# Kernel optimization log

Hardware: AMD Instinct MI355X
Metric: run time of the kernel (lower is better)

Reference implementation:

```python
import jax, jax.numpy as jnp
import numpy as np

N = 50000      # nodes
E = 800000     # edges
H = 64         # hidden_dim
T = 32         # max_node_types
G = 256        # graphs in batch
EPS = 1e-5


def gcn_conv(x, src, dst, W, b, n):
    # GCNConv: transform, add self-loops, symmetric deg normalization, scatter-sum
    x = x @ W  # [N, C]
    loops = jnp.arange(n)
    row = jnp.concatenate([src, loops])
    col = jnp.concatenate([dst, loops])
    deg = jax.ops.segment_sum(jnp.ones_like(col, dtype=x.dtype), col, num_segments=n)
    dinv = jnp.where(deg > 0, jax.lax.rsqrt(deg), 0.0)
    norm = dinv[row] * dinv[col]  # [E+N]
    out = jax.ops.segment_sum(x[row] * norm[:, None], col, num_segments=n)
    return out + b


def batchnorm(x, gamma, beta):
    mean = x.mean(axis=0)
    var = x.var(axis=0)
    return (x - mean) * jax.lax.rsqrt(var + EPS) * gamma + beta


def setup_inputs() -> dict:
    key = jax.random.key(0)
    ks = jax.random.split(key, 24)
    s = 0.05
    nrm = lambda k, shape: (jax.random.normal(k, shape, dtype=jnp.float32) * s)
    inp = {
        "type_ids": jax.random.randint(ks[0], (N,), 0, T),
        "c": jax.random.normal(ks[1], (N,), dtype=jnp.float32),
        "gm": jax.random.normal(ks[2], (N,), dtype=jnp.float32),
        "pos": jax.random.normal(ks[3], (N,), dtype=jnp.float32),
        "r": jax.random.normal(ks[4], (N,), dtype=jnp.float32),
        "vid": jax.random.normal(ks[5], (N,), dtype=jnp.float32),
        "edge_index": jax.random.randint(ks[6], (2, E), 0, N),
        "batch_idx": jnp.sort(jax.random.randint(ks[7], (N,), 0, G)),
        "W1": nrm(ks[8], (T, H)), "b1": jnp.zeros((H,), jnp.float32),
        "W2": nrm(ks[9], (5, H)), "b2": jnp.zeros((H,), jnp.float32),
        "Wg0": nrm(ks[10], (2 * H, H)), "bg0": jnp.zeros((H,), jnp.float32),
        "Wg1": nrm(ks[11], (H, H)), "bg1": jnp.zeros((H,), jnp.float32),
        "Wg2": nrm(ks[12], (H, H)), "bg2": jnp.zeros((H,), jnp.float32),
        "gam0": jnp.ones((H,), jnp.float32), "bet0": jnp.zeros((H,), jnp.float32),
        "gam1": jnp.ones((H,), jnp.float32), "bet1": jnp.zeros((H,), jnp.float32),
        "Wout": nrm(ks[13], (H, 4)), "bout": jnp.zeros((4,), jnp.float32),
    }
    return inp


def reference(type_ids, c, gm, pos, r, vid, edge_index, batch_idx,
              W1, b1, W2, b2, Wg0, bg0, Wg1, bg1, Wg2, bg2,
              gam0, bet0, gam1, bet1, Wout, bout):
    # OneHot embedding branch
    x_t = jax.nn.one_hot(type_ids, T, dtype=jnp.float32) @ W1 + b1   # [N, H]
    x_num = jnp.stack([c, gm, pos, r, vid], axis=-1) @ W2 + b2       # [N, H]
    z = jnp.concatenate([x_t, x_num], axis=-1)                       # [N, 2H]
    src, dst = edge_index[0], edge_index[1]
    # GCN (PyG BasicGNN): conv -> bn -> relu for first L-1 layers, last conv bare
    z = gcn_conv(z, src, dst, Wg0, bg0, N)
    z = jax.nn.relu(batchnorm(z, gam0, bet0))
    z = gcn_conv(z, src, dst, Wg1, bg1, N)
    z = jax.nn.relu(batchnorm(z, gam1, bet1))
    z = gcn_conv(z, src, dst, Wg2, bg2, N)
    # outer activation
    z = jax.nn.relu(z)
    # global_mean_pool over batch index
    sums = jax.ops.segment_sum(z, batch_idx, num_segments=G)
    counts = jax.ops.segment_sum(jnp.ones((N,), jnp.float32), batch_idx, num_segments=G)
    pooled = sums / jnp.maximum(counts, 1.0)[:, None]                # [G, H]
    return pooled @ Wout + bout                                      # [G, 4]
```

## Files before the change

### kernel.cpp

```cpp
#include <hip/hip_runtime.h>
#include <hip/hip_bf16.h>


__device__ __forceinline__ unsigned short f2bf(float f) {
    unsigned int x = (unsigned int)__float_as_int(f);
    x += 0x7fffu + ((x >> 16) & 1u);
    return (unsigned short)(x >> 16);
}

#define CONV_BLOCKS 1024

__global__ void precompute_mats(const float* __restrict__ W1, const float* __restrict__ b1,
                                const float* __restrict__ W2, const float* __restrict__ b2,
                                const float* __restrict__ Wg0,
                                float* __restrict__ M1, float* __restrict__ M2,
                                float* __restrict__ cvec, int T) {
    int tid = threadIdx.x;
    for (int idx = tid; idx < T * 64; idx += blockDim.x) {
        int t = idx >> 6, c = idx & 63;
        float a = 0.f;
        for (int k = 0; k < 64; ++k) a += W1[t * 64 + k] * Wg0[k * 64 + c];
        M1[idx] = a;
    }
    for (int idx = tid; idx < 5 * 64; idx += blockDim.x) {
        int j = idx >> 6, c = idx & 63;
        float a = 0.f;
        for (int k = 0; k < 64; ++k) a += W2[j * 64 + k] * Wg0[(64 + k) * 64 + c];
        M2[idx] = a;
    }
    for (int c = tid; c < 64; c += blockDim.x) {
        float a = 0.f;
        for (int k = 0; k < 64; ++k)
            a += b1[k] * Wg0[k * 64 + c] + b2[k] * Wg0[(64 + k) * 64 + c];
        cvec[c] = a;
    }
}

__global__ void node_embed(const int* __restrict__ type_ids,
                           const float* __restrict__ f0, const float* __restrict__ f1,
                           const float* __restrict__ f2, const float* __restrict__ f3,
                           const float* __restrict__ f4,
                           const float* __restrict__ M1, const float* __restrict__ M2,
                           const float* __restrict__ cvec, const float* __restrict__ dinv,
                           unsigned short* __restrict__ hb, int n) {
    int i = blockIdx.x * (blockDim.x >> 6) + (threadIdx.x >> 6);
    int lane = threadIdx.x & 63;
    if (i >= n) return;
    int t = type_ids[i];
    float a = M1[t * 64 + lane] + cvec[lane];
    a += f0[i] * M2[0 * 64 + lane];
    a += f1[i] * M2[1 * 64 + lane];
    a += f2[i] * M2[2 * 64 + lane];
    a += f3[i] * M2[3 * 64 + lane];
    a += f4[i] * M2[4 * 64 + lane];
    hb[((unsigned)i << 6) | lane] = f2bf(a * dinv[i]);
}

__global__ void count_deg(const int* __restrict__ dst, int* __restrict__ deg, int e) {
    int i = blockIdx.x * blockDim.x + threadIdx.x;
    if (i < e) atomicAdd(&deg[dst[i]], 1);
}

#define SCAN_TILE 1024
__global__ void scan_local(const int* __restrict__ deg, int* __restrict__ loc,
                           int* __restrict__ tilesum, float* __restrict__ dinv, int n) {
    __shared__ int wsum[16];
    __shared__ int wexcl[16];
    const int tid = threadIdx.x;
    const int lane = tid & 63, w = tid >> 6;
    int i = blockIdx.x * SCAN_TILE + tid;
    int v = (i < n) ? deg[i] : 0;
    if (i < n) dinv[i] = rsqrtf((float)(v + 1));
    int incl = v;
#pragma unroll
    for (int ofs = 1; ofs < 64; ofs <<= 1) {
        int t = __shfl_up(incl, (unsigned)ofs, 64);
        if (lane >= ofs) incl += t;
    }
    if (lane == 63) wsum[w] = incl;
    __syncthreads();
    if (w == 0 && lane < 16) {
        int s = wsum[lane];
        int sc = s;
#pragma unroll
        for (int ofs = 1; ofs < 16; ofs <<= 1) {
            int t = __shfl_up(sc, (unsigned)ofs, 64);
            if (lane >= ofs) sc += t;
        }
        wexcl[lane] = sc - s;
        if (lane == 15) wsum[15] = sc;
    }
    __syncthreads();
    if (i < n) loc[i] = wexcl[w] + incl;
    if (tid == 0) tilesum[blockIdx.x] = wsum[15];
}

__global__ void scan_tiles(int* __restrict__ tilesum, int* __restrict__ tileoff, int nt) {
    int lane = threadIdx.x;
    int v = (lane < nt) ? tilesum[lane] : 0;
    int incl = v;
#pragma unroll
    for (int ofs = 1; ofs < 64; ofs <<= 1) {
        int t = __shfl_up(incl, (unsigned)ofs, 64);
        if (lane >= ofs) incl += t;
    }
    if (lane < nt) tileoff[lane] = incl - v;
}

__global__ void scan_add(const int* __restrict__ loc, const int* __restrict__ tileoff,
                         int* __restrict__ off, int* __restrict__ cursor, int n) {
    int i = blockIdx.x * blockDim.x + threadIdx.x;
    if (i >= n) return;
    int val = tileoff[i / SCAN_TILE] + loc[i];
    off[i + 1] = val;
    if (i + 1 < n) cursor[i + 1] = val;
    if (i == 0) { off[0] = 0; cursor[0] = 0; }
}

#define NB 64
__global__ void init_buckets(const int* __restrict__ off, int* __restrict__ bkt_cursor,
                             int N) {
    int b = threadIdx.x;
    if (b < NB) bkt_cursor[b] = off[min(b << 10, N)];
}

#define EPB 8192
__global__ void bucket_edges(const int* __restrict__ src, const int* __restrict__ dst,
                             int* __restrict__ bkt_cursor, unsigned* __restrict__ bucketed,
                             int E) {
    __shared__ int hist[NB];
    __shared__ int base_[NB];
    const int t = threadIdx.x;
    int start = blockIdx.x * EPB;
    int end = min(E, start + EPB);
    if (t < NB) hist[t] = 0;
    __syncthreads();
    for (int i = start + t; i < end; i += 256) {
        int b = dst[i] >> 10;
        atomicAdd(&hist[b], 1);
    }
    __syncthreads();
    if (t < NB) {
        base_[t] = atomicAdd(&bkt_cursor[t], hist[t]);
        hist[t] = 0;
    }
    __syncthreads();
    for (int i = start + t; i < end; i += 256) {
        int d = dst[i];
        int b = d >> 10;
        int slot = atomicAdd(&hist[b], 1);
        bucketed[base_[b] + slot] = ((unsigned)src[i] << 16) | (unsigned)d;
    }
}

#define SCAT_SLICES 4
__global__ void scatter_csr(const unsigned* __restrict__ bucketed, const int* __restrict__ off,
                            int* __restrict__ cursor, unsigned short* __restrict__ csr_u,
                            int N) {
    int wg = blockIdx.x;
    int b = wg / SCAT_SLICES, q = wg % SCAT_SLICES;
    int bstart = off[min(b << 10, N)];
    int bend = off[min((b + 1) << 10, N)];
    int cntb = bend - bstart;
    if (cntb == 0) return;
    int per = (cntb + SCAT_SLICES - 1) / SCAT_SLICES;
    int s0 = bstart + q * per;
    int s1 = min(bend, s0 + per);
    for (int i = s0 + (int)threadIdx.x; i < s1; i += 256) {
        unsigned u = bucketed[i];
        int s = (int)(u >> 16);
        int d = (int)(u & 0xffffu);
        int pos = atomicAdd(&cursor[d], 1);
        csr_u[pos] = (unsigned short)s;
    }
}

__global__ void build_graph_off(const int* __restrict__ batch, int* __restrict__ go,
                                int n, int G) {
    int i = blockIdx.x * blockDim.x + threadIdx.x;
    if (i >= n) return;
    int b = batch[i];
    if (i == 0) {
        for (int g = 0; g <= b; ++g) go[g] = 0;
    } else {
        int p = batch[i - 1];
        if (p != b) for (int g = p + 1; g <= b; ++g) go[g] = i;
    }
    if (i == n - 1) {
        for (int g = b + 1; g <= G; ++g) go[g] = n;
    }
}

__device__ __forceinline__ void gather_add(float acc[8], uint4 v) {
    acc[0] += __uint_as_float(v.x << 16);
    acc[1] += __uint_as_float(v.x & 0xffff0000u);
    acc[2] += __uint_as_float(v.y << 16);
    acc[3] += __uint_as_float(v.y & 0xffff0000u);
    acc[4] += __uint_as_float(v.z << 16);
    acc[5] += __uint_as_float(v.z & 0xffff0000u);
    acc[6] += __uint_as_float(v.w << 16);
    acc[7] += __uint_as_float(v.w & 0xffff0000u);
}

__device__ __forceinline__ void reduce8(float acc[8]) {
#pragma unroll
    for (int q = 0; q < 8; ++q) {
        acc[q] += __shfl_xor(acc[q], 8, 64);
        acc[q] += __shfl_xor(acc[q], 16, 64);
        acc[q] += __shfl_xor(acc[q], 32, 64);
    }
}

__device__ __forceinline__ void node_aggregate(float acc[8],
                                               const unsigned short* __restrict__ hb,
                                               const unsigned short* __restrict__ csr_u,
                                               int i, int b, int deg, int N,
                                               int eg, int cc) {
#pragma unroll
    for (int q = 0; q < 8; ++q) acc[q] = 0.f;
    int nb = (deg + 8) >> 3;
#pragma unroll 1
    for (int t = 0; t < nb; t += 4) {
        int j0 = (t << 3) + eg;
        int j1 = j0 + 8, j2 = j0 + 16, j3 = j0 + 24;
        unsigned e0 = csr_u[b + j0 - 1];
        unsigned e1 = csr_u[b + j1 - 1];
        unsigned e2 = csr_u[b + j2 - 1];
        unsigned e3 = csr_u[b + j3 - 1];
        unsigned s0 = (j0 == 0) ? (unsigned)i : ((j0 <= deg) ? e0 : (unsigned)N);
        unsigned s1 = (j1 <= deg) ? e1 : (unsigned)N;
        unsigned s2 = (j2 <= deg) ? e2 : (unsigned)N;
        unsigned s3 = (j3 <= deg) ? e3 : (unsigned)N;
        uint4 v0 = *(const uint4*)&hb[(s0 << 6) + (cc << 3)];
        uint4 v1 = *(const uint4*)&hb[(s1 << 6) + (cc << 3)];
        uint4 v2 = *(const uint4*)&hb[(s2 << 6) + (cc << 3)];
        uint4 v3 = *(const uint4*)&hb[(s3 << 6) + (cc << 3)];
        gather_add(acc, v0);
        gather_add(acc, v1);
        gather_add(acc, v2);
        gather_add(acc, v3);
    }
    reduce8(acc);
}

__device__ __forceinline__ void node_aggregate_pair(float accA[8], float accB[8],
                                                    const unsigned short* __restrict__ hb,
                                                    const unsigned short* __restrict__ csr_u,
                                                    int iA, int bA, int degA,
                                                    int iB, int bB, int degB,
                                                    int N, int eg, int cc) {
#pragma unroll
    for (int q = 0; q < 8; ++q) { accA[q] = 0.f; accB[q] = 0.f; }
    int dmax = max(degA, degB);
    int nb = (dmax + 8) >> 3;
#pragma unroll 1
    for (int t = 0; t < nb; t += 2) {
        int j0 = (t << 3) + eg;
        int j1 = j0 + 8;
        unsigned a0 = csr_u[bA + j0 - 1];
        unsigned a1 = csr_u[bA + j1 - 1];
        unsigned c0 = csr_u[bB + j0 - 1];
        unsigned c1 = csr_u[bB + j1 - 1];
        unsigned sA0 = (j0 == 0) ? (unsigned)iA : ((j0 <= degA) ? a0 : (unsigned)N);
        unsigned sA1 = (j1 <= degA) ? a1 : (unsigned)N;
        unsigned sB0 = (j0 == 0) ? (unsigned)iB : ((j0 <= degB) ? c0 : (unsigned)N);
        unsigned sB1 = (j1 <= degB) ? c1 : (unsigned)N;
        uint4 vA0 = *(const uint4*)&hb[(sA0 << 6) + (cc << 3)];
        uint4 vB0 = *(const uint4*)&hb[(sB0 << 6) + (cc << 3)];
        uint4 vA1 = *(const uint4*)&hb[(sA1 << 6) + (cc << 3)];
        uint4 vB1 = *(const uint4*)&hb[(sB1 << 6) + (cc << 3)];
        gather_add(accA, vA0);
        gather_add(accB, vB0);
        gather_add(accA, vA1);
        gather_add(accB, vB1);
    }
    reduce8(accA);
    reduce8(accB);
}

__global__ __launch_bounds__(256, 2) void conv_gather_bn(
        const unsigned short* __restrict__ hb,
        const int* __restrict__ off, const unsigned short* __restrict__ csr_u,
        const float* __restrict__ dinv, const float* __restrict__ bias,
        float* __restrict__ y, float* __restrict__ partials, int n) {
    __shared__ float sh[4][128];
    const int w = threadIdx.x >> 6;
    const int lane = threadIdx.x & 63;
    const int eg = lane >> 3, cc = lane & 7;
    const int wid = blockIdx.x * 4 + w;
    const int nw = gridDim.x * 4;
    const float4* b4 = (const float4*)bias;
    float4 bb0 = b4[cc * 2], bb1 = b4[cc * 2 + 1];
    float bl[8] = {bb0.x, bb0.y, bb0.z, bb0.w, bb1.x, bb1.y, bb1.z, bb1.w};
    float bsum[8], bsq[8];
#pragma unroll
    for (int q = 0; q < 8; ++q) { bsum[q] = 0.f; bsq[q] = 0.f; }

    for (int iA = wid * 2; iA < n; iA += nw * 2) {
        int iB = iA + 1;
        bool bv = iB < n;
        int iBc = bv ? iB : iA;
        int bA = off[iA], degA = off[iA + 1] - bA;
        int bB = off[iBc], degB = off[iBc + 1] - bB;
        float accA[8], accB[8];
        node_aggregate_pair(accA, accB, hb, csr_u, iA, bA, degA, iBc, bB, degB,
                            n, eg, cc);
        if (eg == 0) {
            float diA = dinv[iA];
            float oA[8];
#pragma unroll
            for (int q = 0; q < 8; ++q) {
                oA[q] = accA[q] * diA + bl[q];
                bsum[q] += oA[q];
                bsq[q] += oA[q] * oA[q];
            }
            float4* o = (float4*)&y[((size_t)iA << 6) + (cc << 3)];
            o[0] = make_float4(oA[0], oA[1], oA[2], oA[3]);
            o[1] = make_float4(oA[4], oA[5], oA[6], oA[7]);
            if (bv) {
                float diB = dinv[iB];
                float oB[8];
#pragma unroll
                for (int q = 0; q < 8; ++q) {
                    oB[q] = accB[q] * diB + bl[q];
                    bsum[q] += oB[q];
                    bsq[q] += oB[q] * oB[q];
                }
                float4* ob = (float4*)&y[((size_t)iB << 6) + (cc << 3)];
                ob[0] = make_float4(oB[0], oB[1], oB[2], oB[3]);
                ob[1] = make_float4(oB[4], oB[5], oB[6], oB[7]);
            }
        }
    }
    if (eg == 0) {
#pragma unroll
        for (int q = 0; q < 8; ++q) {
            sh[w][cc * 8 + q] = bsum[q];
            sh[w][64 + cc * 8 + q] = bsq[q];
        }
    }
    __syncthreads();
    if (threadIdx.x < 128) {
        int t = threadIdx.x;
        partials[blockIdx.x * 128 + t] = sh[0][t] + sh[1][t] + sh[2][t] + sh[3][t];
    }
}

#define POOL_SLICES 16
__global__ __launch_bounds__(256, 2) void conv_relu_pool(
        const unsigned short* __restrict__ hb,
        const int* __restrict__ off, const unsigned short* __restrict__ csr_u,
        const float* __restrict__ dinv, const float* __restrict__ bias,
        const int* __restrict__ go, float* __restrict__ pooled, int n, int G) {
    int wave = blockIdx.x * (blockDim.x >> 6) + (threadIdx.x >> 6);
    int g = wave >> 4, k = wave & (POOL_SLICES - 1);
    if (g >= G) return;
    const int lane = threadIdx.x & 63;
    const int eg = lane >> 3, cc = lane & 7;
    int gs = go[g], ge = go[g + 1];
    int cntg = ge - gs;
    if (cntg == 0) return;
    int per = (cntg + POOL_SLICES - 1) >> 4;
    int s0 = gs + k * per;
    int s1 = min(ge, s0 + per);
    if (s0 >= s1) return;
    const float4* b4 = (const float4*)bias;
    float4 bb0 = b4[cc * 2], bb1 = b4[cc * 2 + 1];
    float bl[8] = {bb0.x, bb0.y, bb0.z, bb0.w, bb1.x, bb1.y, bb1.z, bb1.w};
    float accp[8];
#pragma unroll
    for (int q = 0; q < 8; ++q) accp[q] = 0.f;
    int i = s0;
    for (; i + 1 < s1; i += 2) {
        int bA = off[i], degA = off[i + 1] - bA;
        int bB = off[i + 1], degB = off[i + 2] - bB;
        float accA[8], accB[8];
        node_aggregate_pair(accA, accB, hb, csr_u, i, bA, degA, i + 1, bB, degB,
                            n, eg, cc);
        float diA = dinv[i], diB = dinv[i + 1];
#pragma unroll
        for (int q = 0; q < 8; ++q) {
            accp[q] += fmaxf(accA[q] * diA + bl[q], 0.f);
            accp[q] += fmaxf(accB[q] * diB + bl[q], 0.f);
        }
    }
    if (i < s1) {
        int b = off[i], deg = off[i + 1] - b;
        float acc[8];
        node_aggregate(acc, hb, csr_u, i, b, deg, n, eg, cc);
        float di = dinv[i];
#pragma unroll
        for (int q = 0; q < 8; ++q) accp[q] += fmaxf(acc[q] * di + bl[q], 0.f);
    }
    atomicAdd(&pooled[g * 64 + (cc << 3) + eg], accp[eg]);
}

__global__ __launch_bounds__(1024) void bn_finalize(const float* __restrict__ partials, int nblk,
                            const float* __restrict__ gamma, const float* __restrict__ beta,
                            float* __restrict__ scsh, int n) {
    __shared__ float red[8][128];
    __shared__ float tot[128];
    int t = threadIdx.x;
    int ch = t & 127, sl = t >> 7;
    float a = 0.f;
#pragma unroll 8
    for (int b = sl; b < nblk; b += 8) a += partials[b * 128 + ch];
    red[sl][ch] = a;
    __syncthreads();
    if (t < 128) {
        float s = 0.f;
#pragma unroll
        for (int i = 0; i < 8; ++i) s += red[i][t];
        tot[t] = s;
    }
    __syncthreads();
    if (t < 64) {
        float mean = tot[t] / (float)n;
        float var = tot[64 + t] / (float)n - mean * mean;
        float sc = rsqrtf(var + 1e-5f) * gamma[t];
        scsh[t] = sc;
        scsh[64 + t] = beta[t] - mean * sc;
    }
}

struct alignas(16) us8 { unsigned short v[8]; };
__global__ __launch_bounds__(256, 2) void bn_relu_gemm(const float* __restrict__ y,
                             const float* __restrict__ scsh, const float* __restrict__ W,
                             const float* __restrict__ dinv,
                             unsigned short* __restrict__ hb, int n) {
    __shared__ float4 yt4[128 * 16];
    __shared__ float4 wt4[64 * 16];
    float* wt = (float*)wt4;
    const int t = threadIdx.x;
    const int base = blockIdx.x * 128;

    const float4* W4 = (const float4*)W;
#pragma unroll
    for (int i = 0; i < 4; ++i) {
        int g = t + 256 * i;
        int k = g >> 4;
        int c0 = (g & 15) << 2;
        float4 wv = W4[g];
        float wvf[4] = {wv.x, wv.y, wv.z, wv.w};
#pragma unroll
        for (int j = 0; j < 4; ++j) {
            int c = c0 + j;
            wt[c * 64 + (((k >> 2) ^ ((c >> 2) & 15)) << 2) + (k & 3)] = wvf[j];
        }
    }
    const float4* y4 = (const float4*)y;
#pragma unroll
    for (int i = 0; i < 8; ++i) {
        int g = t + 256 * i;
        int r = g >> 4, kc = g & 15;
        int row = base + r;
        float4 v = make_float4(0.f, 0.f, 0.f, 0.f);
        if (row < n) v = y4[(size_t)row * 16 + kc];
        int c0 = kc << 2;
        v.x = fmaxf(v.x * scsh[c0 + 0] + scsh[64 + c0 + 0], 0.f);
        v.y = fmaxf(v.y * scsh[c0 + 1] + scsh[64 + c0 + 1], 0.f);
        v.z = fmaxf(v.z * scsh[c0 + 2] + scsh[64 + c0 + 2], 0.f);
        v.w = fmaxf(v.w * scsh[c0 + 3] + scsh[64 + c0 + 3], 0.f);
        yt4[r * 16 + (kc ^ ((r >> 2) & 15))] = v;
    }
    __syncthreads();

    const int w = t >> 6;
    const int lane = t & 63;
    const int ng = lane >> 3;
    const int cg = lane & 7;
    const int rl = w * 32 + ng * 4;
    const int c0 = cg * 8;
    const int sa = (rl >> 2) & 15;
    float acc[4][8];
#pragma unroll
    for (int m = 0; m < 4; ++m)
#pragma unroll
        for (int j = 0; j < 8; ++j) acc[m][j] = 0.f;

#pragma unroll 1
    for (int kc = 0; kc < 16; ++kc) {
        float4 a[4];
#pragma unroll
        for (int m = 0; m < 4; ++m) a[m] = yt4[(rl + m) * 16 + (kc ^ sa)];
#pragma unroll
        for (int j = 0; j < 8; ++j) {
            int c = c0 + j;
            float4 b = wt4[c * 16 + (kc ^ ((c >> 2) & 15))];
#pragma unroll
            for (int m = 0; m < 4; ++m)
                acc[m][j] += a[m].x * b.x + a[m].y * b.y +
                             a[m].z * b.z + a[m].w * b.w;
        }
    }

#pragma unroll
    for (int m = 0; m < 4; ++m) {
        int row = base + rl + m;
        if (row < n) {
            float dv = dinv[row];
            us8 p;
#pragma unroll
            for (int j = 0; j < 8; ++j) p.v[j] = f2bf(acc[m][j] * dv);
            *(us8*)&hb[((size_t)row << 6) | c0] = p;
        }
    }
}

__global__ void final_out(const float* __restrict__ pooled, const int* __restrict__ go,
                          const float* __restrict__ Wout, const float* __restrict__ bout,
                          float* __restrict__ out, int G) {
    int idx = blockIdx.x * blockDim.x + threadIdx.x;
    if (idx >= G * 4) return;
    int g = idx >> 2, o = idx & 3;
    float inv = 1.f / fmaxf((float)(go[g + 1] - go[g]), 1.f);
    float a = 0.f;
    for (int k = 0; k < 64; ++k) a += pooled[g * 64 + k] * Wout[k * 4 + o];
    out[idx] = a * inv + bout[o];
}

extern "C" void kernel_launch(void* const* d_in, const int* in_sizes, int n_in,
                              void* d_out, int out_size, void* d_ws, size_t ws_size,
                              hipStream_t stream) {
    const int N = in_sizes[0];
    const int E = in_sizes[6] / 2;
    const int T = in_sizes[8] / 64;
    const int G = out_size / 4;

    const int*   type_ids = (const int*)d_in[0];
    const float* fc   = (const float*)d_in[1];
    const float* fgm  = (const float*)d_in[2];
    const float* fpos = (const float*)d_in[3];
    const float* fr   = (const float*)d_in[4];
    const float* fvid = (const float*)d_in[5];
    const int*   ei   = (const int*)d_in[6];
    const int*   batch = (const int*)d_in[7];
    const float* W1 = (const float*)d_in[8];
    const float* b1 = (const float*)d_in[9];
    const float* W2 = (const float*)d_in[10];
    const float* b2 = (const float*)d_in[11];
    const float* Wg0 = (const float*)d_in[12];
    const float* bg0 = (const float*)d_in[13];
    const float* Wg1 = (const float*)d_in[14];
    const float* bg1 = (const float*)d_in[15];
    const float* Wg2 = (const float*)d_in[16];
    const float* bg2 = (const float*)d_in[17];
    const float* gam0 = (const float*)d_in[18];
    const float* bet0 = (const float*)d_in[19];
    const float* gam1 = (const float*)d_in[20];
    const float* bet1 = (const float*)d_in[21];
    const float* Wout = (const float*)d_in[22];
    const float* bout = (const float*)d_in[23];

    const int* e_src = ei;
    const int* e_dst = ei + E;

    char* ws = (char*)d_ws;
    size_t o = 0;
    auto alloc = [&](size_t bytes) -> char* {
        char* p = ws + o;
        o += (bytes + 255) & ~(size_t)255;
        return p;
    };
    const int NTILES = (N + SCAN_TILE - 1) / SCAN_TILE;
    unsigned short* hb = (unsigned short*)alloc((size_t)(N + 1) * 64 * 2);
    float* y        = (float*)alloc((size_t)N * 64 * 4);
    int*   deg      = (int*)alloc((size_t)N * 4);
    float* dinv     = (float*)alloc((size_t)N * 4);
    int*   off      = (int*)alloc((size_t)(N + 1) * 4);
    int*   cursor   = (int*)alloc((size_t)N * 4);
    int*   loc      = (int*)alloc((size_t)N * 4);
    int*   tilesum  = (int*)alloc((size_t)NTILES * 4);
    int*   tileoff  = (int*)alloc((size_t)NTILES * 4);
    unsigned short* csrBuf = (unsigned short*)alloc(((size_t)E + 160) * 2);
    unsigned short* csr_u  = csrBuf + 1;
    unsigned* bucketed = (unsigned*)alloc((size_t)E * 4);
    int*   bkt_cursor  = (int*)alloc(NB * 4);
    int*   go       = (int*)alloc((size_t)(G + 1) * 4);
    float* part0    = (float*)alloc((size_t)CONV_BLOCKS * 128 * 4);
    float* part1    = (float*)alloc((size_t)CONV_BLOCKS * 128 * 4);
    float* scsh0    = (float*)alloc(128 * 4);
    float* scsh1    = (float*)alloc(128 * 4);
    float* pooled   = (float*)alloc((size_t)G * 64 * 4);
    float* M1       = (float*)alloc((size_t)T * 64 * 4);
    float* M2       = (float*)alloc(5 * 64 * 4);
    float* cvec     = (float*)alloc(64 * 4);
    (void)ws_size;

    hipMemsetAsync(deg, 0, (size_t)N * 4, stream);
    hipMemsetAsync(csrBuf, 0, 2, stream);
    hipMemsetAsync(csr_u + E, 0, 128 * 2, stream);
    hipMemsetAsync(hb + (size_t)N * 64, 0, 128, stream);
    hipMemsetAsync(pooled, 0, (size_t)G * 64 * 4, stream);

    const int waves_per_blk = 4;
    const int nblk_nodes = (N + waves_per_blk - 1) / waves_per_blk;
    const int nblk_gemm = (N + 127) / 128;
    const int nb_used = (N + 1023) >> 10;

    count_deg<<<(E + 255) / 256, 256, 0, stream>>>(e_dst, deg, E);
    scan_local<<<NTILES, SCAN_TILE, 0, stream>>>(deg, loc, tilesum, dinv, N);
    scan_tiles<<<1, 64, 0, stream>>>(tilesum, tileoff, NTILES);
    scan_add<<<(N + 255) / 256, 256, 0, stream>>>(loc, tileoff, off, cursor, N);
    init_buckets<<<1, 64, 0, stream>>>(off, bkt_cursor, N);
    bucket_edges<<<(E + EPB - 1) / EPB, 256, 0, stream>>>(e_src, e_dst, bkt_cursor,
                                                          bucketed, E);
    scatter_csr<<<nb_used * SCAT_SLICES, 256, 0, stream>>>(bucketed, off, cursor, csr_u, N);
    build_graph_off<<<(N + 255) / 256, 256, 0, stream>>>(batch, go, N, G);

    precompute_mats<<<1, 256, 0, stream>>>(W1, b1, W2, b2, Wg0, M1, M2, cvec, T);
    node_embed<<<nblk_nodes, 256, 0, stream>>>(type_ids, fc, fgm, fpos, fr, fvid,
                                               M1, M2, cvec, dinv, hb, N);

    conv_gather_bn<<<CONV_BLOCKS, 256, 0, stream>>>(hb, off, csr_u, dinv, bg0, y, part0, N);
    bn_finalize<<<1, 1024, 0, stream>>>(part0, CONV_BLOCKS, gam0, bet0, scsh0, N);
    bn_relu_gemm<<<nblk_gemm, 256, 0, stream>>>(y, scsh0, Wg1, dinv, hb, N);

    conv_gather_bn<<<CONV_BLOCKS, 256, 0, stream>>>(hb, off, csr_u, dinv, bg1, y, part1, N);
    bn_finalize<<<1, 1024, 0, stream>>>(part1, CONV_BLOCKS, gam1, bet1, scsh1, N);
    bn_relu_gemm<<<nblk_gemm, 256, 0, stream>>>(y, scsh1, Wg2, dinv, hb, N);

    {
        int waves = G * POOL_SLICES;
        int blocks = (waves + waves_per_blk - 1) / waves_per_blk;
        conv_relu_pool<<<blocks, 256, 0, stream>>>(hb, off, csr_u, dinv, bg2, go,
                                                   pooled, N, G);
    }

    final_out<<<(G * 4 + 255) / 256, 256, 0, stream>>>(pooled, go, Wout, bout, (float*)d_out, G);
}
```

Measured before the change: 284.1 us.

## Build CSR via bucket histogram and per-bucket LDS counting sort

Replaces the global per-node degree atomics and multi-kernel prefix scan with a bucket-level histogram and scan over 64 buckets. Degrees, offsets, dinv and CSR placement are then computed inside each bucket's workgroup using shared-memory counters. This drops several kernel launches, the N-sized memset and the global atomics on cursor. The cost is one workgroup per bucket (about 49 blocks) doing all the per-bucket work, which limits parallelism in the finalize step.

```diff
diff --git a/kernel.cpp b/kernel.cpp
--- a/kernel.cpp
+++ b/kernel.cpp
@@ -9,6 +9,8 @@
 }
 
 #define CONV_BLOCKS 1024
+#define NB 64
+#define EPB 8192
 
 __global__ void precompute_mats(const float* __restrict__ W1, const float* __restrict__ b1,
                                 const float* __restrict__ W2, const float* __restrict__ b2,
@@ -56,75 +58,32 @@
     hb[((unsigned)i << 6) | lane] = f2bf(a * dinv[i]);
 }
 
-__global__ void count_deg(const int* __restrict__ dst, int* __restrict__ deg, int e) {
-    int i = blockIdx.x * blockDim.x + threadIdx.x;
-    if (i < e) atomicAdd(&deg[dst[i]], 1);
-}
-
-#define SCAN_TILE 1024
-__global__ void scan_local(const int* __restrict__ deg, int* __restrict__ loc,
-                           int* __restrict__ tilesum, float* __restrict__ dinv, int n) {
-    __shared__ int wsum[16];
-    __shared__ int wexcl[16];
-    const int tid = threadIdx.x;
-    const int lane = tid & 63, w = tid >> 6;
-    int i = blockIdx.x * SCAN_TILE + tid;
-    int v = (i < n) ? deg[i] : 0;
-    if (i < n) dinv[i] = rsqrtf((float)(v + 1));
+__global__ void hist_buckets(const int* __restrict__ dst, int* __restrict__ bktcnt, int E) {
+    __shared__ int h[NB];
+    const int t = threadIdx.x;
+    if (t < NB) h[t] = 0;
+    __syncthreads();
+    int start = blockIdx.x * EPB, end = min(E, start + EPB);
+    for (int i = start + t; i < end; i += 256) atomicAdd(&h[dst[i] >> 10], 1);
+    __syncthreads();
+    if (t < NB && h[t]) atomicAdd(&bktcnt[t], h[t]);
+}
+
+__global__ void scan_buckets(const int* __restrict__ bktcnt, int* __restrict__ bkt_base,
+                             int* __restrict__ bkt_cursor, int E) {
+    int lane = threadIdx.x;
+    int v = bktcnt[lane];
     int incl = v;
 #pragma unroll
     for (int ofs = 1; ofs < 64; ofs <<= 1) {
         int t = __shfl_up(incl, (unsigned)ofs, 64);
         if (lane >= ofs) incl += t;
     }
-    if (lane == 63) wsum[w] = incl;
-    __syncthreads();
-    if (w == 0 && lane < 16) {
-        int s = wsum[lane];
-        int sc = s;
-#pragma unroll
-        for (int ofs = 1; ofs < 16; ofs <<= 1) {
-            int t = __shfl_up(sc, (unsigned)ofs, 64);
-            if (lane >= ofs) sc += t;
-        }
-        wexcl[lane] = sc - s;
-        if (lane == 15) wsum[15] = sc;
-    }
-    __syncthreads();
-    if (i < n) loc[i] = wexcl[w] + incl;
-    if (tid == 0) tilesum[blockIdx.x] = wsum[15];
-}
-
-__global__ void scan_tiles(int* __restrict__ tilesum, int* __restrict__ tileoff, int nt) {
-    int lane = threadIdx.x;
-    int v = (lane < nt) ? tilesum[lane] : 0;
-    int incl = v;
-#pragma unroll
-    for (int ofs = 1; ofs < 64; ofs <<= 1) {
-        int t = __shfl_up(incl, (unsigned)ofs, 64);
-        if (lane >= ofs) incl += t;
-    }
-    if (lane < nt) tileoff[lane] = incl - v;
-}
-
-__global__ void scan_add(const int* __restrict__ loc, const int* __restrict__ tileoff,
-                         int* __restrict__ off, int* __restrict__ cursor, int n) {
-    int i = blockIdx.x * blockDim.x + threadIdx.x;
-    if (i >= n) return;
-    int val = tileoff[i / SCAN_TILE] + loc[i];
-    off[i + 1] = val;
-    if (i + 1 < n) cursor[i + 1] = val;
-    if (i == 0) { off[0] = 0; cursor[0] = 0; }
-}
-
-#define NB 64
-__global__ void init_buckets(const int* __restrict__ off, int* __restrict__ bkt_cursor,
-                             int N) {
-    int b = threadIdx.x;
-    if (b < NB) bkt_cursor[b] = off[min(b << 10, N)];
-}
-
-#define EPB 8192
+    bkt_base[lane] = incl - v;
+    bkt_cursor[lane] = incl - v;
+    if (lane == 63) bkt_base[64] = E;
+}
+
 __global__ void bucket_edges(const int* __restrict__ src, const int* __restrict__ dst,
                              int* __restrict__ bkt_cursor, unsigned* __restrict__ bucketed,
                              int E) {
@@ -141,7 +100,7 @@
     }
     __syncthreads();
     if (t < NB) {
-        base_[t] = atomicAdd(&bkt_cursor[t], hist[t]);
+        base_[t] = hist[t] ? atomicAdd(&bkt_cursor[t], hist[t]) : 0;
         hist[t] = 0;
     }
     __syncthreads();
@@ -153,25 +112,59 @@
     }
 }
 
-#define SCAT_SLICES 4
-__global__ void scatter_csr(const unsigned* __restrict__ bucketed, const int* __restrict__ off,
-                            int* __restrict__ cursor, unsigned short* __restrict__ csr_u,
-                            int N) {
-    int wg = blockIdx.x;
-    int b = wg / SCAT_SLICES, q = wg % SCAT_SLICES;
-    int bstart = off[min(b << 10, N)];
-    int bend = off[min((b + 1) << 10, N)];
-    int cntb = bend - bstart;
-    if (cntb == 0) return;
-    int per = (cntb + SCAT_SLICES - 1) / SCAT_SLICES;
-    int s0 = bstart + q * per;
-    int s1 = min(bend, s0 + per);
-    for (int i = s0 + (int)threadIdx.x; i < s1; i += 256) {
+__global__ __launch_bounds__(256) void bucket_finalize(
+        const unsigned* __restrict__ bucketed, const int* __restrict__ bkt_base,
+        unsigned short* __restrict__ csr_u, int* __restrict__ off,
+        float* __restrict__ dinv, int N, int E) {
+    __shared__ int cnt[1024];
+    __shared__ int ex[1024];
+    __shared__ int wsum[4];
+    const int b = blockIdx.x;
+    const int t = threadIdx.x;
+    const int base = bkt_base[b], end = bkt_base[b + 1];
+    for (int l = t; l < 1024; l += 256) cnt[l] = 0;
+    __syncthreads();
+    for (int i = base + t; i < end; i += 256) {
         unsigned u = bucketed[i];
-        int s = (int)(u >> 16);
-        int d = (int)(u & 0xffffu);
-        int pos = atomicAdd(&cursor[d], 1);
-        csr_u[pos] = (unsigned short)s;
+        atomicAdd(&cnt[u & 1023], 1);
+    }
+    __syncthreads();
+    int c0 = cnt[t * 4 + 0], c1 = cnt[t * 4 + 1], c2 = cnt[t * 4 + 2], c3 = cnt[t * 4 + 3];
+    int s = c0 + c1 + c2 + c3;
+    const int lane = t & 63, w = t >> 6;
+    int incl = s;
+#pragma unroll
+    for (int ofs = 1; ofs < 64; ofs <<= 1) {
+        int tv = __shfl_up(incl, (unsigned)ofs, 64);
+        if (lane >= ofs) incl += tv;
+    }
+    if (lane == 63) wsum[w] = incl;
+    __syncthreads();
+    int wofs = 0;
+#pragma unroll
+    for (int k = 0; k < 4; ++k) wofs += (k < w) ? wsum[k] : 0;
+    int excl = wofs + incl - s;
+    ex[t * 4 + 0] = excl;
+    ex[t * 4 + 1] = excl + c0;
+    ex[t * 4 + 2] = excl + c0 + c1;
+    ex[t * 4 + 3] = excl + c0 + c1 + c2;
+    __syncthreads();
+    const int i0 = b << 10;
+    for (int l = t; l < 1024; l += 256) {
+        int i = i0 + l;
+        if (i < N) {
+            off[i] = base + ex[l];
+            dinv[i] = rsqrtf((float)(cnt[l] + 1));
+        }
+    }
+    if (b == 0 && t == 0) off[N] = E;
+    __syncthreads();
+    for (int l = t; l < 1024; l += 256) cnt[l] = ex[l];
+    __syncthreads();
+    for (int i = base + t; i < end; i += 256) {
+        unsigned u = bucketed[i];
+        int pos = base + atomicAdd(&cnt[u & 1023], 1);
+        csr_u[pos] = (unsigned short)(u >> 16);
     }
 }
 
@@ -562,20 +555,16 @@
         o += (bytes + 255) & ~(size_t)255;
         return p;
     };
-    const int NTILES = (N + SCAN_TILE - 1) / SCAN_TILE;
     unsigned short* hb = (unsigned short*)alloc((size_t)(N + 1) * 64 * 2);
     float* y        = (float*)alloc((size_t)N * 64 * 4);
-    int*   deg      = (int*)alloc((size_t)N * 4);
     float* dinv     = (float*)alloc((size_t)N * 4);
     int*   off      = (int*)alloc((size_t)(N + 1) * 4);
-    int*   cursor   = (int*)alloc((size_t)N * 4);
-    int*   loc      = (int*)alloc((size_t)N * 4);
-    int*   tilesum  = (int*)alloc((size_t)NTILES * 4);
-    int*   tileoff  = (int*)alloc((size_t)NTILES * 4);
     unsigned short* csrBuf = (unsigned short*)alloc(((size_t)E + 160) * 2);
     unsigned short* csr_u  = csrBuf + 1;
     unsigned* bucketed = (unsigned*)alloc((size_t)E * 4);
-    int*   bkt_cursor  = (int*)alloc(NB * 4);
+    int*   bktcnt   = (int*)alloc(NB * 4);
+    int*   bkt_base = (int*)alloc((NB + 1) * 4);
+    int*   bkt_cursor = (int*)alloc(NB * 4);
     int*   go       = (int*)alloc((size_t)(G + 1) * 4);
     float* part0    = (float*)alloc((size_t)CONV_BLOCKS * 128 * 4);
     float* part1    = (float*)alloc((size_t)CONV_BLOCKS * 128 * 4);
@@ -587,7 +576,7 @@
     float* cvec     = (float*)alloc(64 * 4);
     (void)ws_size;
 
-    hipMemsetAsync(deg, 0, (size_t)N * 4, stream);
+    hipMemsetAsync(bktcnt, 0, NB * 4, stream);
     hipMemsetAsync(csrBuf, 0, 2, stream);
     hipMemsetAsync(csr_u + E, 0, 128 * 2, stream);
     hipMemsetAsync(hb + (size_t)N * 64, 0, 128, stream);
@@ -598,14 +587,12 @@
     const int nblk_gemm = (N + 127) / 128;
     const int nb_used = (N + 1023) >> 10;
 
-    count_deg<<<(E + 255) / 256, 256, 0, stream>>>(e_dst, deg, E);
-    scan_local<<<NTILES, SCAN_TILE, 0, stream>>>(deg, loc, tilesum, dinv, N);
-    scan_tiles<<<1, 64, 0, stream>>>(tilesum, tileoff, NTILES);
-    scan_add<<<(N + 255) / 256, 256, 0, stream>>>(loc, tileoff, off, cursor, N);
-    init_buckets<<<1, 64, 0, stream>>>(off, bkt_cursor, N);
+    hist_buckets<<<(E + EPB - 1) / EPB, 256, 0, stream>>>(e_dst, bktcnt, E);
+    scan_buckets<<<1, 64, 0, stream>>>(bktcnt, bkt_base, bkt_cursor, E);
     bucket_edges<<<(E + EPB - 1) / EPB, 256, 0, stream>>>(e_src, e_dst, bkt_cursor,
                                                           bucketed, E);
-    scatter_csr<<<nb_used * SCAT_SLICES, 256, 0, stream>>>(bucketed, off, cursor, csr_u, N);
+    bucket_finalize<<<nb_used, 256, 0, stream>>>(bucketed, bkt_base, csr_u, off,
+                                                 dinv, N, E);
     build_graph_off<<<(N + 255) / 256, 256, 0, stream>>>(batch, go, N, G);
 
     precompute_mats<<<1, 256, 0, stream>>>(W1, b1, W2, b2, Wg0, M1, M2, cvec, T);
```

Result: faster. 254.8 us (-10.3%).
